# Kernel tuning notes

Measured on AMD Instinct MI355X. Metric: run time of the kernel, lower is better.

Reference implementation:

```python
import jax, jax.numpy as jnp
import numpy as np

T, B, IN, H = 512, 4096, 1, 12

def setup_inputs() -> dict:
    key = jax.random.key(0)
    ks = jax.random.split(key, 7)
    s = 1.0 / np.sqrt(H)
    return {
        "X": jax.random.normal(ks[0], (T, B, IN), dtype=jnp.float32),
        "W_ih": jax.random.uniform(ks[1], (4 * H, IN), minval=-s, maxval=s, dtype=jnp.float32),
        "W_hh": jax.random.uniform(ks[2], (4 * H, H), minval=-s, maxval=s, dtype=jnp.float32),
        "b_ih": jax.random.uniform(ks[3], (4 * H,), minval=-s, maxval=s, dtype=jnp.float32),
        "b_hh": jax.random.uniform(ks[4], (4 * H,), minval=-s, maxval=s, dtype=jnp.float32),
        "fc_w": jax.random.uniform(ks[5], (1, H), minval=-s, maxval=s, dtype=jnp.float32),
        "fc_b": jax.random.uniform(ks[6], (1,), minval=-s, maxval=s, dtype=jnp.float32),
    }

def reference(X, W_ih, W_hh, b_ih, b_hh, fc_w, fc_b):
    # Precompute input contribution for all timesteps: [T, B, 4H]
    x_proj = jnp.einsum('tbi,gi->tbg', X, W_ih) + b_ih + b_hh
    h0 = jnp.zeros((X.shape[1], H), dtype=X.dtype)
    c0 = jnp.zeros_like(h0)

    def step(carry, xp_t):
        h, c = carry
        gates = xp_t + h @ W_hh.T  # [B, 4H]
        i, f, g, o = jnp.split(gates, 4, axis=-1)  # PyTorch gate order i,f,g,o
        i = jax.nn.sigmoid(i)
        f = jax.nn.sigmoid(f)
        g = jnp.tanh(g)
        o = jax.nn.sigmoid(o)
        c_new = f * c + i * g
        h_new = o * jnp.tanh(c_new)
        return (h_new, c_new), h_new

    _, hs = jax.lax.scan(step, (h0, c0), x_proj)  # hs: [T, B, H]
    return jnp.einsum('tbh,oh->tbo', hs, fc_w) + fc_b  # [T, B, 1]
```

## Files before the change

kernel.cpp:

```cpp
#include <hip/hip_runtime.h>


#define TT    512
#define NB    4096
#define HH    12
#define RPW   4
#define CHUNK 64
#define XPAD  68

typedef float v2f __attribute__((ext_vector_type(2)));

static __device__ __forceinline__ v2f pkfma(v2f a, v2f b, v2f c) {
#if __has_builtin(__builtin_elementwise_fma)
    return __builtin_elementwise_fma(a, b, c);
#else
    v2f r; r.x = fmaf(a.x, b.x, c.x); r.y = fmaf(a.y, b.y, c.y); return r;
#endif
}

#define SNEG (-1.44269504088896340736f)
#define SPOS ( 2.88539008177792681472f)

#define ROR(r) (0x120 + (r))

__global__ __launch_bounds__(64, 1)
void lstm_fused(const float* __restrict__ X,
                const float* __restrict__ W_ih,
                const float* __restrict__ W_hh,
                const float* __restrict__ b_ih,
                const float* __restrict__ b_hh,
                const float* __restrict__ fc_w,
                const float* __restrict__ fc_b,
                float* __restrict__ out)
{
    __shared__ float xchunk[RPW][XPAD];

    const int lane = threadIdx.x;
    const int row  = lane >> 4;
    const int j    = lane & 15;
    const int cellbase = blockIdx.x * RPW;
    const int cell = cellbase + row;

    int sid[16];
    sid[0] = j;
#define PROBE(r) sid[r] = __builtin_amdgcn_update_dpp(0, j, ROR(r), 0xF, 0xF, true);
    PROBE(1)  PROBE(2)  PROBE(3)  PROBE(4)  PROBE(5)
    PROBE(6)  PROBE(7)  PROBE(8)  PROBE(9)  PROBE(10)
    PROBE(11) PROBE(12) PROBE(13) PROBE(14) PROBE(15)
#undef PROBE

    const int jc = (j < HH) ? j : (HH - 1);
    v2f wifU[16], wgoU[16];
    #pragma unroll
    for (int r = 0; r < 16; ++r) {
        const int  s  = sid[r];
        const int  sc = (s < HH) ? s : (HH - 1);
        const float g = ((j >= HH) || (s < HH)) ? 1.0f : 0.0f;
        wifU[r].x = g * SNEG * W_hh[(0 * HH + jc) * HH + sc];
        wifU[r].y = g * SNEG * W_hh[(1 * HH + jc) * HH + sc];
        wgoU[r].x = g * SPOS * W_hh[(2 * HH + jc) * HH + sc];
        wgoU[r].y = g * SNEG * W_hh[(3 * HH + jc) * HH + sc];
    }
    v2f bif, bgo, wxif, wxgo;
    bif.x  = SNEG * (b_ih[0 * HH + jc] + b_hh[0 * HH + jc]);
    bif.y  = SNEG * (b_ih[1 * HH + jc] + b_hh[1 * HH + jc]);
    bgo.x  = SPOS * (b_ih[2 * HH + jc] + b_hh[2 * HH + jc]);
    bgo.y  = SNEG * (b_ih[3 * HH + jc] + b_hh[3 * HH + jc]);
    wxif.x = SNEG * W_ih[0 * HH + jc];
    wxif.y = SNEG * W_ih[1 * HH + jc];
    wxgo.x = SPOS * W_ih[2 * HH + jc];
    wxgo.y = SNEG * W_ih[3 * HH + jc];
    const float fcb  = fc_b[0];
    const float fcwj = (j < HH) ? fc_w[j] : 0.0f;

    float cst = 0.0f;
    float hn  = 0.0f;
    int hbits = 0;

    float4 gq = *(const float4*)(X + (size_t)lane * NB + cellbase);

    for (int tc = 0; tc < TT; tc += CHUNK) {
        xchunk[0][lane] = gq.x;
        xchunk[1][lane] = gq.y;
        xchunk[2][lane] = gq.z;
        xchunk[3][lane] = gq.w;
        if (tc + CHUNK < TT)
            gq = *(const float4*)(X + (size_t)(tc + CHUNK + lane) * NB + cellbase);

        for (int t4 = 0; t4 < CHUNK; t4 += 4) {
            const float4 xq = *(const float4*)&xchunk[row][t4];
            const float xs[4] = {xq.x, xq.y, xq.z, xq.w};

            #pragma unroll
            for (int u = 0; u < 4; ++u) {
                v2f gifA = bif, goA = bgo;
                v2f gifB; gifB.x = 0.0f; gifB.y = 0.0f;
                v2f goB;  goB.x  = 0.0f; goB.y  = 0.0f;
                {
                    v2f hk; hk.x = hn; hk.y = hn;
                    gifA = pkfma(wifU[0], hk, gifA);
                    goA  = pkfma(wgoU[0], hk, goA);
                }
#define XR(r) { \
                const int hr_##r = __builtin_amdgcn_update_dpp(0, hbits, ROR(r), 0xF, 0xF, true); \
                const float hf = __int_as_float(hr_##r); \
                v2f hk; hk.x = hf; hk.y = hf; \
                if ((r) < 8) { gifA = pkfma(wifU[r], hk, gifA); goA = pkfma(wgoU[r], hk, goA); } \
                else         { gifB = pkfma(wifU[r], hk, gifB); goB = pkfma(wgoU[r], hk, goB); } }
                XR(1)  XR(2)  XR(3)  XR(4)  XR(5)
                XR(6)  XR(7)  XR(8)  XR(9)  XR(10)
                XR(11) XR(12) XR(13) XR(14) XR(15)
#undef XR
                v2f gif = gifA + gifB;
                v2f ggo = goA + goB;
                v2f xvv; xvv.x = xs[u]; xvv.y = xs[u];
                gif = pkfma(xvv, wxif, gif);
                ggo = pkfma(xvv, wxgo, ggo);

                const float si = __builtin_amdgcn_rcpf(1.0f + __builtin_amdgcn_exp2f(gif.x));
                const float sf = __builtin_amdgcn_rcpf(1.0f + __builtin_amdgcn_exp2f(gif.y));
                const float rg = __builtin_amdgcn_rcpf(1.0f + __builtin_amdgcn_exp2f(ggo.x));
                const float so = __builtin_amdgcn_rcpf(1.0f + __builtin_amdgcn_exp2f(ggo.y));
                const float tg = fmaf(-2.0f, rg, 1.0f);
                cst = fmaf(sf, cst, si * tg);
                const float rc   = __builtin_amdgcn_rcpf(1.0f + __builtin_amdgcn_exp2f(SPOS * cst));
                const float m2so = -2.0f * so;
                hn    = fmaf(m2so, rc, so);
                hbits = __float_as_int(hn);

                float p = hn * fcwj;
                p += __int_as_float(__builtin_amdgcn_update_dpp(0, __float_as_int(p), ROR(8), 0xF, 0xF, true));
                p += __int_as_float(__builtin_amdgcn_update_dpp(0, __float_as_int(p), ROR(4), 0xF, 0xF, true));
                p += __int_as_float(__builtin_amdgcn_update_dpp(0, __float_as_int(p), ROR(2), 0xF, 0xF, true));
                p += __int_as_float(__builtin_amdgcn_update_dpp(0, __float_as_int(p), ROR(1), 0xF, 0xF, true));
                if (j == 0) out[(size_t)(tc + t4 + u) * NB + cell] = p + fcb;
            }
        }
    }
}

extern "C" void kernel_launch(void* const* d_in, const int* in_sizes, int n_in,
                              void* d_out, int out_size, void* d_ws, size_t ws_size,
                              hipStream_t stream) {
    const float* X    = (const float*)d_in[0];
    const float* W_ih = (const float*)d_in[1];
    const float* W_hh = (const float*)d_in[2];
    const float* b_ih = (const float*)d_in[3];
    const float* b_hh = (const float*)d_in[4];
    const float* fc_w = (const float*)d_in[5];
    const float* fc_b = (const float*)d_in[6];
    float* out = (float*)d_out;

    const int grid = NB / RPW;
    lstm_fused<<<grid, 64, 0, stream>>>(X, W_ih, W_hh, b_ih, b_hh, fc_w, fc_b, out);
}
```

Baseline: 182.8 us.

## Defer FC reduction one step and shorten LSTM recurrence critical path

Software-pipelines the per-step output projection: the DPP reduction and store for step t are interleaved into step t+1, filling latency gaps around the transcendental ops. The input-projection FMA moves to the start of the accumulation, off the serial tail. The cell state is kept pre-scaled by the tanh exponent factor, which removes one multiply from the recurrence. The next LDS x-vector is prefetched one group ahead. The cost is extra live registers and an epilogue that flushes the last pending output.

```diff
diff --git a/kernel.cpp b/kernel.cpp
--- a/kernel.cpp
+++ b/kernel.cpp
@@ -18,8 +18,9 @@
 #endif
 }
 
-#define SNEG (-1.44269504088896340736f)
-#define SPOS ( 2.88539008177792681472f)
+#define SNEG   (-1.44269504088896340736f)
+#define SPOS   ( 2.88539008177792681472f)
+#define M2SPOS (-5.77078016355585362944f)
 
 #define ROR(r) (0x120 + (r))
 
@@ -73,9 +74,13 @@
     const float fcb  = fc_b[0];
     const float fcwj = (j < HH) ? fc_w[j] : 0.0f;
 
-    float cst = 0.0f;
-    float hn  = 0.0f;
+    float c2 = 0.0f;
+    float hn = 0.0f;
     int hbits = 0;
+
+    float pPend = 0.0f;
+    unsigned offPrev = 0;
+    float* const outp = out + cell;
 
     float4 gq = *(const float4*)(X + (size_t)lane * NB + cellbase);
 
@@ -87,13 +92,19 @@
         if (tc + CHUNK < TT)
             gq = *(const float4*)(X + (size_t)(tc + CHUNK + lane) * NB + cellbase);
 
+        float4 xq_next = *(const float4*)&xchunk[row][0];
+
         for (int t4 = 0; t4 < CHUNK; t4 += 4) {
-            const float4 xq = *(const float4*)&xchunk[row][t4];
+            const float4 xq = xq_next;
+            const int nx = (t4 + 4 < CHUNK) ? (t4 + 4) : t4;
+            xq_next = *(const float4*)&xchunk[row][nx];
             const float xs[4] = {xq.x, xq.y, xq.z, xq.w};
 
             #pragma unroll
             for (int u = 0; u < 4; ++u) {
-                v2f gifA = bif, goA = bgo;
+                v2f xvv; xvv.x = xs[u]; xvv.y = xs[u];
+                v2f gifA = pkfma(xvv, wxif, bif);
+                v2f goA  = pkfma(xvv, wxgo, bgo);
                 v2f gifB; gifB.x = 0.0f; gifB.y = 0.0f;
                 v2f goB;  goB.x  = 0.0f; goB.y  = 0.0f;
                 {
@@ -111,31 +122,49 @@
                 XR(6)  XR(7)  XR(8)  XR(9)  XR(10)
                 XR(11) XR(12) XR(13) XR(14) XR(15)
 #undef XR
-                v2f gif = gifA + gifB;
-                v2f ggo = goA + goB;
-                v2f xvv; xvv.x = xs[u]; xvv.y = xs[u];
-                gif = pkfma(xvv, wxif, gif);
-                ggo = pkfma(xvv, wxgo, ggo);
+                const v2f gif = gifA + gifB;
+                const v2f ggo = goA + goB;
 
-                const float si = __builtin_amdgcn_rcpf(1.0f + __builtin_amdgcn_exp2f(gif.x));
-                const float sf = __builtin_amdgcn_rcpf(1.0f + __builtin_amdgcn_exp2f(gif.y));
-                const float rg = __builtin_amdgcn_rcpf(1.0f + __builtin_amdgcn_exp2f(ggo.x));
-                const float so = __builtin_amdgcn_rcpf(1.0f + __builtin_amdgcn_exp2f(ggo.y));
-                const float tg = fmaf(-2.0f, rg, 1.0f);
-                cst = fmaf(sf, cst, si * tg);
-                const float rc   = __builtin_amdgcn_rcpf(1.0f + __builtin_amdgcn_exp2f(SPOS * cst));
+                const float Ei = __builtin_amdgcn_exp2f(gif.x);
+                const float Ef = __builtin_amdgcn_exp2f(gif.y);
+                const float Eg = __builtin_amdgcn_exp2f(ggo.x);
+                const float Eo = __builtin_amdgcn_exp2f(ggo.y);
+
+                float p = pPend;
+                p += __int_as_float(__builtin_amdgcn_update_dpp(0, __float_as_int(p), ROR(8), 0xF, 0xF, true));
+                p += __int_as_float(__builtin_amdgcn_update_dpp(0, __float_as_int(p), ROR(4), 0xF, 0xF, true));
+
+                const float si = __builtin_amdgcn_rcpf(1.0f + Ei);
+                const float sf = __builtin_amdgcn_rcpf(1.0f + Ef);
+                const float rg = __builtin_amdgcn_rcpf(1.0f + Eg);
+                const float so = __builtin_amdgcn_rcpf(1.0f + Eo);
+
+                const float tgS = fmaf(M2SPOS, rg, SPOS);
+                c2 = fmaf(sf, c2, si * tgS);
+                const float Ec = __builtin_amdgcn_exp2f(c2);
+
+                p += __int_as_float(__builtin_amdgcn_update_dpp(0, __float_as_int(p), ROR(2), 0xF, 0xF, true));
+                p += __int_as_float(__builtin_amdgcn_update_dpp(0, __float_as_int(p), ROR(1), 0xF, 0xF, true));
+                if (j == 0) *(float*)((char*)outp + offPrev) = p + fcb;
+
+                const float rc   = __builtin_amdgcn_rcpf(1.0f + Ec);
                 const float m2so = -2.0f * so;
                 hn    = fmaf(m2so, rc, so);
                 hbits = __float_as_int(hn);
 
-                float p = hn * fcwj;
-                p += __int_as_float(__builtin_amdgcn_update_dpp(0, __float_as_int(p), ROR(8), 0xF, 0xF, true));
-                p += __int_as_float(__builtin_amdgcn_update_dpp(0, __float_as_int(p), ROR(4), 0xF, 0xF, true));
-                p += __int_as_float(__builtin_amdgcn_update_dpp(0, __float_as_int(p), ROR(2), 0xF, 0xF, true));
-                p += __int_as_float(__builtin_amdgcn_update_dpp(0, __float_as_int(p), ROR(1), 0xF, 0xF, true));
-                if (j == 0) out[(size_t)(tc + t4 + u) * NB + cell] = p + fcb;
+                pPend   = hn * fcwj;
+                offPrev = (unsigned)(tc + t4 + u) << 14;
             }
         }
+    }
+
+    {
+        float p = pPend;
+        p += __int_as_float(__builtin_amdgcn_update_dpp(0, __float_as_int(p), ROR(8), 0xF, 0xF, true));
+        p += __int_as_float(__builtin_amdgcn_update_dpp(0, __float_as_int(p), ROR(4), 0xF, 0xF, true));
+        p += __int_as_float(__builtin_amdgcn_update_dpp(0, __float_as_int(p), ROR(2), 0xF, 0xF, true));
+        p += __int_as_float(__builtin_amdgcn_update_dpp(0, __float_as_int(p), ROR(1), 0xF, 0xF, true));
+        if (j == 0) *(float*)((char*)outp + offPrev) = p + fcb;
     }
 }
 
```

New measurement: 182.2 us. Within noise of the previous version (-0.3%).
